# Optimization experiments

Hardware: AMD Instinct MI355X
Metric: run time of the kernel (lower is better)

The kernel has to match this reference:

```python
import jax, jax.numpy as jnp
import numpy as np

CH = 128
DQK = CH // 8  # 16


def setup_inputs() -> dict:
    key = jax.random.key(0)
    ks = jax.random.split(key, 8)
    B, H, W, C = 4, 64, 64, CH
    inputs = jax.random.normal(ks[0], (B, H, W, C), dtype=jnp.float32)
    # 1x1 conv weights == dense over channel dim
    wq = jax.random.normal(ks[1], (C, DQK), dtype=jnp.float32) * (1.0 / np.sqrt(C))
    bq = jnp.zeros((DQK,), dtype=jnp.float32)
    wk = jax.random.normal(ks[2], (C, DQK), dtype=jnp.float32) * (1.0 / np.sqrt(C))
    bk = jnp.zeros((DQK,), dtype=jnp.float32)
    wv = jax.random.normal(ks[3], (C, C), dtype=jnp.float32) * (1.0 / np.sqrt(C))
    bv = jnp.zeros((C,), dtype=jnp.float32)
    gamma = jnp.zeros((1,), dtype=jnp.float32)
    return {"inputs": inputs, "wq": wq, "bq": bq, "wk": wk, "bk": bk,
            "wv": wv, "bv": bv, "gamma": gamma}


def reference(inputs, wq, bq, wk, bk, wv, bv, gamma):
    B, H, W, C = inputs.shape
    N = H * W
    x = inputs.reshape(B, N, C)  # flatten spatial
    q = x @ wq + bq              # [B, N, d]
    k = x @ wk + bk              # [B, N, d]
    v = x @ wv + bv              # [B, N, C]
    # full N x N attention (no scaling, per SAGAN source)
    scores = jnp.einsum('bnd,bmd->bnm', q, k)
    attn = jax.nn.softmax(scores, axis=-1)
    out = jnp.einsum('bnm,bmc->bnc', attn, v).reshape(B, H, W, C)
    return gamma * out + inputs
```

## Files before the change

### kernel.cpp

```cpp
#include <hip/hip_runtime.h>
#include <hip/hip_bf16.h>


typedef __attribute__((ext_vector_type(4)))  short short4v;
typedef __attribute__((ext_vector_type(8)))  short short8;
typedef __attribute__((ext_vector_type(16))) float f32x16;
typedef unsigned short u16;

#define LOG2E 1.4426950408889634f

__device__ __forceinline__ u16 f2bf(float f) {
  __hip_bfloat16 h = __float2bfloat16(f);
  return __builtin_bit_cast(u16, h);
}
__device__ __forceinline__ u16 f2bf_fast(float f) {
  unsigned u = __builtin_bit_cast(unsigned, f) + 0x8000u;
  return (u16)(u >> 16);
}
__device__ __forceinline__ float bf2f(u16 u) {
  unsigned v = (unsigned)u << 16;
  return __builtin_bit_cast(float, v);
}
__device__ __forceinline__ float fexp2(float x) {
#if __has_builtin(__builtin_amdgcn_exp2f)
  return __builtin_amdgcn_exp2f(x);
#else
  return exp2f(x);
#endif
}
__device__ __forceinline__ unsigned pkbf(float lo, float hi) {
  unsigned a = __builtin_bit_cast(unsigned, lo) + 0x8000u;
  unsigned b = __builtin_bit_cast(unsigned, hi) + 0x8000u;
  unsigned r;
  asm("v_perm_b32 %0, %1, %2, %3" : "=v"(r) : "v"(b), "v"(a), "s"(0x07060302u));
  return r;
}
__device__ __forceinline__ float xhalf_sum(float x) {
  float a = x, b = x;
  asm("v_permlane32_swap_b32 %0, %1" : "+v"(a), "+v"(b));
  return a + b;
}

__global__ __launch_bounds__(256) void qkv_proj(
    const float* __restrict__ x,
    const float* __restrict__ wq, const float* __restrict__ bq,
    const float* __restrict__ wk, const float* __restrict__ bk,
    const float* __restrict__ wv, const float* __restrict__ bv,
    u16* __restrict__ Qb, u16* __restrict__ Kb, u16* __restrict__ Vt)
{
  __shared__ u16 xs[128 * 136];
  __shared__ u16 ws[160 * 136];
  const int tid  = threadIdx.x;
  const int b    = blockIdx.x >> 6;
  const int n0   = ((blockIdx.x >> 1) & 31) * 128;
  const int half = blockIdx.x & 1;

  const float4* xg = (const float4*)(x + ((size_t)b * 4096 + n0) * 128);
#pragma unroll
  for (int p = 0; p < 16; ++p) {
    int idx = tid + p * 256;
    float4 v = xg[idx];
    int n = idx >> 5, i4 = idx & 31;
    short4v pk;
    pk[0] = (short)f2bf(v.x); pk[1] = (short)f2bf(v.y);
    pk[2] = (short)f2bf(v.z); pk[3] = (short)f2bf(v.w);
    *(short4v*)(xs + n * 136 + i4 * 4) = pk;
  }
  if (half == 0) {
#pragma unroll
    for (int p = 0; p < 8; ++p) {
      int idx = tid + p * 256;
      int k = idx >> 4, d = idx & 15;
      ws[d * 136 + k]        = f2bf(wq[idx] * LOG2E);
      ws[(16 + d) * 136 + k] = f2bf(wk[idx]);
    }
#pragma unroll
    for (int p = 0; p < 32; ++p) {
      int idx = tid + p * 256;
      int k = idx >> 6, c = idx & 63;
      ws[(32 + c) * 136 + k] = f2bf(wv[k * 128 + c]);
    }
  } else {
#pragma unroll
    for (int p = 0; p < 32; ++p) {
      int idx = tid + p * 256;
      int k = idx >> 6, c = 64 + (idx & 63);
      ws[(32 + c) * 136 + k] = f2bf(wv[k * 128 + c]);
    }
  }
  __syncthreads();

  const int lane = tid & 63, wid = tid >> 6;
  const int ln31 = lane & 31, hi = lane >> 5;
  const int NJ = half ? 2 : 3;

#pragma unroll 1
  for (int j = 0; j < NJ; ++j) {
    int t = wid + j * 4;
    int mt, nt;
    if (half == 0) { mt = t / 3; nt = t % 3; }
    else           { mt = t >> 1; nt = 3 + (t & 1); }
    const u16* arow = xs + (mt * 32 + ln31) * 136 + hi * 8;
    const u16* brow = ws + (nt * 32 + ln31) * 136 + hi * 8;
    f32x16 acc = (f32x16)0.0f;
#pragma unroll
    for (int ks = 0; ks < 8; ++ks) {
      short8 a = *(const short8*)(arow + ks * 16);
      short8 w = *(const short8*)(brow + ks * 16);
      acc = __builtin_amdgcn_mfma_f32_32x32x16_bf16(a, w, acc, 0, 0, 0);
    }
    if (nt == 0) {
      float bias = (ln31 < 16) ? bq[ln31] * LOG2E : bk[ln31 & 15];
      u16* base = ((ln31 < 16) ? Qb : Kb)
                + ((size_t)b * 4096 + n0 + mt * 32) * 16 + (ln31 & 15);
#pragma unroll
      for (int r = 0; r < 16; ++r) {
        int nl = (r & 3) + 8 * (r >> 2) + 4 * hi;
        base[nl * 16] = f2bf(acc[r] + bias);
      }
    } else {
      int c = (nt - 1) * 32 + ln31;
      float bias = bv[c];
      u16* vb = Vt + ((size_t)b * 128 + c) * 4096 + n0 + mt * 32 + 4 * hi;
#pragma unroll
      for (int g = 0; g < 4; ++g) {
        short4v pk;
        pk[0] = (short)f2bf(acc[g*4+0] + bias);
        pk[1] = (short)f2bf(acc[g*4+1] + bias);
        pk[2] = (short)f2bf(acc[g*4+2] + bias);
        pk[3] = (short)f2bf(acc[g*4+3] + bias);
        *(short4v*)(vb + 8 * g) = pk;
      }
    }
  }
}

template<int NKS>
__global__ __launch_bounds__(256, 3) void attn(
    const u16* __restrict__ Qb, const u16* __restrict__ Kb,
    const u16* __restrict__ Vt,
    u16* __restrict__ Ob, float* __restrict__ Lp)
{
  __shared__ __align__(16) char sm[2][18432];
  const int tid  = threadIdx.x;
  const int lane = tid & 63;
  const int wid  = tid >> 6;
  const int ln31 = lane & 31;
  const int hi   = lane >> 5;

  const int bx   = blockIdx.x;
  const int ks   = bx % NKS;
  const int rest = bx / NKS;
  const int b    = rest >> 5;
  const int qt   = rest & 31;
  const int qw   = qt * 128 + wid * 32;
  const int c0   = (ks * 64) / NKS;
  const int c1   = ((ks + 1) * 64) / NKS;

  const short8 qf = *(const short8*)(Qb + (((size_t)b * 4096 + qw + ln31) << 4) + (hi << 3));

  f32x16 acc[4];
#pragma unroll
  for (int ct = 0; ct < 4; ++ct) acc[ct] = (f32x16)0.0f;
  float lacc = 0.f;
  const f32x16 cbias = (f32x16)(-16.0f);

  const char* vg = (const char*)(Vt + (size_t)b * 128 * 4096);
  const char* kg = (const char*)(Kb + (size_t)b * 4096 * 16);
  const int vc = tid >> 1;
  const int vp = tid & 1;

  uint4 rv0, rv1, rv2, rv3;
  uint4 rkc0, rkc1, rkn0, rkn1;

  auto loadV = [&](int kb) {
    const char* vs = vg + (size_t)vc * 8192 + (size_t)kb * 2 + vp * 64;
    rv0 = *(const uint4*)(vs);
    rv1 = *(const uint4*)(vs + 16);
    rv2 = *(const uint4*)(vs + 32);
    rv3 = *(const uint4*)(vs + 48);
  };
  auto loadK = [&](int kb, uint4& k0, uint4& k1) {
    const char* kr = kg + (size_t)(kb + ln31) * 32 + hi * 16;
    k0 = *(const uint4*)(kr);
    k1 = *(const uint4*)(kr + 1024);
  };
  auto storeV = [&](char* buf) {
    char* vd = buf + vc * 144 + vp * 64;
    *(uint4*)(vd)      = rv0;
    *(uint4*)(vd + 16) = rv1;
    *(uint4*)(vd + 32) = rv2;
    *(uint4*)(vd + 48) = rv3;
  };

  auto compute = [&](const char* buf, uint4 k0, uint4 k1) {
#pragma unroll
    for (int kt = 0; kt < 2; ++kt) {
      short8 kf = __builtin_bit_cast(short8, kt ? k1 : k0);
      f32x16 s = __builtin_amdgcn_mfma_f32_32x32x16_bf16(kf, qf, cbias, 0, 0, 0);

      float e0 = fexp2(s[0]),  e1 = fexp2(s[1]);
      unsigned u0 = pkbf(e0, e1);  float t0 = e0 + e1;
      float e2 = fexp2(s[2]),  e3 = fexp2(s[3]);
      unsigned u1 = pkbf(e2, e3);  float t1 = e2 + e3;
      float e4 = fexp2(s[4]),  e5 = fexp2(s[5]);
      unsigned u2 = pkbf(e4, e5);  float t2 = e4 + e5;
      float e6 = fexp2(s[6]),  e7 = fexp2(s[7]);
      unsigned u3 = pkbf(e6, e7);  float t3 = e6 + e7;
      float e8 = fexp2(s[8]),  e9 = fexp2(s[9]);
      unsigned y0 = pkbf(e8, e9);  float t4 = e8 + e9;
      float ea = fexp2(s[10]), eb = fexp2(s[11]);
      unsigned y1 = pkbf(ea, eb);  float t5 = ea + eb;
      float ec = fexp2(s[12]), ed = fexp2(s[13]);
      unsigned y2 = pkbf(ec, ed);  float t6 = ec + ed;
      float ee = fexp2(s[14]), ef = fexp2(s[15]);
      unsigned y3 = pkbf(ee, ef);  float t7 = ee + ef;
      lacc += ((t0 + t1) + (t2 + t3)) + ((t4 + t5) + (t6 + t7));

      asm("v_permlane32_swap_b32 %0, %1" : "+v"(u0), "+v"(u2));
      asm("v_permlane32_swap_b32 %0, %1" : "+v"(u1), "+v"(u3));
      asm("v_permlane32_swap_b32 %0, %1" : "+v"(y0), "+v"(y2));
      asm("v_permlane32_swap_b32 %0, %1" : "+v"(y1), "+v"(y3));
      union { unsigned u[4]; short8 s8; } pa0, pa1;
      pa0.u[0] = u0; pa0.u[1] = u1; pa0.u[2] = u2; pa0.u[3] = u3;
      pa1.u[0] = y0; pa1.u[1] = y1; pa1.u[2] = y2; pa1.u[3] = y3;

      __builtin_amdgcn_s_setprio(1);
#pragma unroll
      for (int ct = 0; ct < 4; ++ct) {
        const char* vrow = buf + (ct * 32 + ln31) * 144 + kt * 64 + hi * 16;
        short8 vf0 = *(const short8*)(vrow);
        short8 vf1 = *(const short8*)(vrow + 32);
        acc[ct] = __builtin_amdgcn_mfma_f32_32x32x16_bf16(pa0.s8, vf0, acc[ct], 0, 0, 0);
        acc[ct] = __builtin_amdgcn_mfma_f32_32x32x16_bf16(pa1.s8, vf1, acc[ct], 0, 0, 0);
      }
      __builtin_amdgcn_s_setprio(0);
    }
  };

  loadV(c0 * 64);
  loadK(c0 * 64, rkc0, rkc1);
  storeV(sm[0]);
  __syncthreads();
  int cur = 0;
#pragma unroll 1
  for (int it = c0; it < c1; ++it) {
    if (it < c1 - 1) {
      loadV((it + 1) * 64);
      loadK((it + 1) * 64, rkn0, rkn1);
    }
    compute(sm[cur], rkc0, rkc1);
    if (it < c1 - 1) storeV(sm[cur ^ 1]);
    __syncthreads();
    rkc0 = rkn0; rkc1 = rkn1; cur ^= 1;
  }

  float lt = xhalf_sum(lacc);
  if (lane < 32)
    Lp[(size_t)ks * 16384 + (size_t)b * 4096 + qw + lane] = lt;
  u16* Op = Ob + ((size_t)ks * 16384 + (size_t)b * 4096 + qw) * 128;
#pragma unroll
  for (int ct = 0; ct < 4; ++ct) {
#pragma unroll
    for (int r = 0; r < 16; ++r) {
      int q = (r & 3) + 8 * (r >> 2) + 4 * hi;
      Op[(size_t)q * 128 + ct * 32 + ln31] = f2bf_fast(acc[ct][r]);
    }
  }
}

template<int NKS>
__global__ __launch_bounds__(256) void combine(
    const u16* __restrict__ Ob, const float* __restrict__ Lp,
    const float* __restrict__ x, const float* __restrict__ gamma,
    float* __restrict__ out)
{
  int i    = blockIdx.x * 256 + threadIdx.x;
  int nrow = i >> 4;
  int c0   = (i & 15) << 3;

  float wsum = 0.f;
#pragma unroll
  for (int p = 0; p < NKS; ++p) wsum += Lp[(size_t)p * 16384 + nrow];
  float inv = gamma[0] / wsum;

  size_t off = (size_t)nrow * 128 + c0;
  float accv[8];
#pragma unroll
  for (int j = 0; j < 8; ++j) accv[j] = 0.f;
#pragma unroll
  for (int p = 0; p < NKS; ++p) {
    short8 v = *(const short8*)(Ob + (size_t)p * 16384 * 128 + off);
#pragma unroll
    for (int j = 0; j < 8; ++j) accv[j] += bf2f((u16)v[j]);
  }
  float4 xa = *(const float4*)(x + off);
  float4 xb = *(const float4*)(x + off + 4);
  float4 ra, rb;
  ra.x = fmaf(accv[0], inv, xa.x); ra.y = fmaf(accv[1], inv, xa.y);
  ra.z = fmaf(accv[2], inv, xa.z); ra.w = fmaf(accv[3], inv, xa.w);
  rb.x = fmaf(accv[4], inv, xb.x); rb.y = fmaf(accv[5], inv, xb.y);
  rb.z = fmaf(accv[6], inv, xb.z); rb.w = fmaf(accv[7], inv, xb.w);
  *(float4*)(out + off)     = ra;
  *(float4*)(out + off + 4) = rb;
}

extern "C" void kernel_launch(void* const* d_in, const int* in_sizes, int n_in,
                              void* d_out, int out_size, void* d_ws, size_t ws_size,
                              hipStream_t stream)
{
  const float* x  = (const float*)d_in[0];
  const float* wq = (const float*)d_in[1];
  const float* bq = (const float*)d_in[2];
  const float* wk = (const float*)d_in[3];
  const float* bk = (const float*)d_in[4];
  const float* wv = (const float*)d_in[5];
  const float* bv = (const float*)d_in[6];
  const float* gm = (const float*)d_in[7];

  char* w = (char*)d_ws;
  u16*   Qb = (u16*)(w);
  u16*   Kb = (u16*)(w + (512ll << 10));
  u16*   Vt = (u16*)(w + (1ll << 20));
  u16*   Ob = (u16*)(w + (5ll << 20));
  float* out = (float*)d_out;

  qkv_proj<<<256, 256, 0, stream>>>(x, wq, bq, wk, bk, wv, bv, Qb, Kb, Vt);

  const size_t need6 = (5ll << 20) + 6ll * (4ll << 20) + 6ll * 16384 * 4;
  if (ws_size >= need6) {
    float* Lp = (float*)(w + (5ll << 20) + 6ll * (4ll << 20));
    attn<6><<<768, 256, 0, stream>>>(Qb, Kb, Vt, Ob, Lp);
    combine<6><<<1024, 256, 0, stream>>>(Ob, Lp, x, gm, out);
  } else {
    float* Lp = (float*)(w + (5ll << 20) + 2ll * (4ll << 20));
    attn<2><<<256, 256, 0, stream>>>(Qb, Kb, Vt, Ob, Lp);
    combine<2><<<1024, 256, 0, stream>>>(Ob, Lp, x, gm, out);
  }
}
```

Measured before the change: 47.28 us.

## Software-pipeline softmax P computation one iteration ahead of PV MFMAs

Result: no change. 46.40 us (-1.9%).

```diff
diff --git a/kernel.cpp b/kernel.cpp
--- a/kernel.cpp
+++ b/kernel.cpp
@@ -171,7 +171,8 @@
   const int vp = tid & 1;
 
   uint4 rv0, rv1, rv2, rv3;
-  uint4 rkc0, rkc1, rkn0, rkn1;
+  uint4 rk0, rk1;
+  short8 paA0, paA1, paB0, paB1;
 
   auto loadV = [&](int kb) {
     const char* vs = vg + (size_t)vc * 8192 + (size_t)kb * 2 + vp * 64;
@@ -180,10 +181,10 @@
     rv2 = *(const uint4*)(vs + 32);
     rv3 = *(const uint4*)(vs + 48);
   };
-  auto loadK = [&](int kb, uint4& k0, uint4& k1) {
+  auto loadK = [&](int kb) {
     const char* kr = kg + (size_t)(kb + ln31) * 32 + hi * 16;
-    k0 = *(const uint4*)(kr);
-    k1 = *(const uint4*)(kr + 1024);
+    rk0 = *(const uint4*)(kr);
+    rk1 = *(const uint4*)(kr + 1024);
   };
   auto storeV = [&](char* buf) {
     char* vd = buf + vc * 144 + vp * 64;
@@ -193,10 +194,10 @@
     *(uint4*)(vd + 48) = rv3;
   };
 
-  auto compute = [&](const char* buf, uint4 k0, uint4 k1) {
+  auto computeP = [&]() {
 #pragma unroll
     for (int kt = 0; kt < 2; ++kt) {
-      short8 kf = __builtin_bit_cast(short8, kt ? k1 : k0);
+      short8 kf = __builtin_bit_cast(short8, kt ? rk1 : rk0);
       f32x16 s = __builtin_amdgcn_mfma_f32_32x32x16_bf16(kf, qf, cbias, 0, 0, 0);
 
       float e0 = fexp2(s[0]),  e1 = fexp2(s[1]);
@@ -221,38 +222,50 @@
       asm("v_permlane32_swap_b32 %0, %1" : "+v"(u1), "+v"(u3));
       asm("v_permlane32_swap_b32 %0, %1" : "+v"(y0), "+v"(y2));
       asm("v_permlane32_swap_b32 %0, %1" : "+v"(y1), "+v"(y3));
-      union { unsigned u[4]; short8 s8; } pa0, pa1;
-      pa0.u[0] = u0; pa0.u[1] = u1; pa0.u[2] = u2; pa0.u[3] = u3;
-      pa1.u[0] = y0; pa1.u[1] = y1; pa1.u[2] = y2; pa1.u[3] = y3;
-
-      __builtin_amdgcn_s_setprio(1);
-#pragma unroll
-      for (int ct = 0; ct < 4; ++ct) {
-        const char* vrow = buf + (ct * 32 + ln31) * 144 + kt * 64 + hi * 16;
-        short8 vf0 = *(const short8*)(vrow);
-        short8 vf1 = *(const short8*)(vrow + 32);
-        acc[ct] = __builtin_amdgcn_mfma_f32_32x32x16_bf16(pa0.s8, vf0, acc[ct], 0, 0, 0);
-        acc[ct] = __builtin_amdgcn_mfma_f32_32x32x16_bf16(pa1.s8, vf1, acc[ct], 0, 0, 0);
-      }
-      __builtin_amdgcn_s_setprio(0);
-    }
+      union { unsigned u[4]; short8 s8; } f0, f1;
+      f0.u[0] = u0; f0.u[1] = u1; f0.u[2] = u2; f0.u[3] = u3;
+      f1.u[0] = y0; f1.u[1] = y1; f1.u[2] = y2; f1.u[3] = y3;
+      if (kt == 0) { paA0 = f0.s8; paA1 = f1.s8; }
+      else         { paB0 = f0.s8; paB1 = f1.s8; }
+    }
+  };
+
+  auto doPV = [&](const char* buf) {
+    __builtin_amdgcn_s_setprio(1);
+#pragma unroll
+    for (int ct = 0; ct < 4; ++ct) {
+      const char* vrow = buf + (ct * 32 + ln31) * 144 + hi * 16;
+      short8 v00 = *(const short8*)(vrow);
+      short8 v01 = *(const short8*)(vrow + 32);
+      short8 v10 = *(const short8*)(vrow + 64);
+      short8 v11 = *(const short8*)(vrow + 96);
+      acc[ct] = __builtin_amdgcn_mfma_f32_32x32x16_bf16(paA0, v00, acc[ct], 0, 0, 0);
+      acc[ct] = __builtin_amdgcn_mfma_f32_32x32x16_bf16(paA1, v01, acc[ct], 0, 0, 0);
+      acc[ct] = __builtin_amdgcn_mfma_f32_32x32x16_bf16(paB0, v10, acc[ct], 0, 0, 0);
+      acc[ct] = __builtin_amdgcn_mfma_f32_32x32x16_bf16(paB1, v11, acc[ct], 0, 0, 0);
+    }
+    __builtin_amdgcn_s_setprio(0);
   };
 
   loadV(c0 * 64);
-  loadK(c0 * 64, rkc0, rkc1);
+  loadK(c0 * 64);
   storeV(sm[0]);
   __syncthreads();
+  computeP();
   int cur = 0;
 #pragma unroll 1
   for (int it = c0; it < c1; ++it) {
     if (it < c1 - 1) {
       loadV((it + 1) * 64);
-      loadK((it + 1) * 64, rkn0, rkn1);
-    }
-    compute(sm[cur], rkc0, rkc1);
-    if (it < c1 - 1) storeV(sm[cur ^ 1]);
-    __syncthreads();
-    rkc0 = rkn0; rkc1 = rkn1; cur ^= 1;
+      loadK((it + 1) * 64);
+    }
+    doPV(sm[cur]);
+    if (it < c1 - 1) {
+      storeV(sm[cur ^ 1]);
+      __syncthreads();
+      computeP();
+    }
+    cur ^= 1;
   }
 
   float lt = xhalf_sum(lacc);
```
